# Performance work log

Hardware: AMD Instinct MI355X
Metric: run time of the kernel (lower is better)

The kernel has to match this reference:

```python
import jax, jax.numpy as jnp
import numpy as np

N_NODES = 20000
N_EDGES = 320000
IN_DIM = 256
HIDDEN = 256
OUT_DIM = 128
N_LAYERS = 3
N_GROUPS = 4
EXP_PER_GROUP = 2
N_EXPERTS = N_GROUPS * EXP_PER_GROUP
TOP_K = 2


def setup_inputs() -> dict:
    key = jax.random.key(0)
    ks = jax.random.split(key, 12)
    d = HIDDEN
    r = 2 * d  # router/expert input dim: concat(node, neighbor-mean)
    x = jax.random.normal(ks[0], (N_NODES, IN_DIM), dtype=jnp.float32)
    edge_index = jax.random.randint(ks[1], (2, N_EDGES), 0, N_NODES, dtype=jnp.int32)
    s = 0.05
    Wg = jax.random.normal(ks[2], (N_LAYERS, r, N_GROUPS), dtype=jnp.float32) * s
    We = jax.random.normal(ks[3], (N_LAYERS, r, N_EXPERTS), dtype=jnp.float32) * s
    Ww = jax.random.normal(ks[4], (N_LAYERS, r, d), dtype=jnp.float32) * s
    W1 = jax.random.normal(ks[5], (N_LAYERS, N_EXPERTS, r, d), dtype=jnp.float32) * s
    b1 = jnp.zeros((N_LAYERS, N_EXPERTS, d), dtype=jnp.float32)
    W2 = jax.random.normal(ks[6], (N_LAYERS, N_EXPERTS, d, d), dtype=jnp.float32) * s
    b2 = jnp.zeros((N_LAYERS, N_EXPERTS, d), dtype=jnp.float32)
    wc = jax.random.normal(ks[7], (N_LAYERS, r, 1), dtype=jnp.float32) * s
    Wout = jax.random.normal(ks[8], (d, OUT_DIM), dtype=jnp.float32) * s
    return {"x": x, "edge_index": edge_index, "Wg": Wg, "We": We, "Ww": Ww,
            "W1": W1, "b1": b1, "W2": W2, "b2": b2, "wc": wc, "Wout": Wout}


def _moe_layer(h, src, dst, deg, Wg, We, Ww, W1, b1, W2, b2, wc):
    N = h.shape[0]
    # graph message passing: mean aggregation over incoming edges
    agg = jax.ops.segment_sum(h[src], dst, num_segments=N) / deg  # [N, d]
    r = jnp.concatenate([h, agg], axis=-1)  # [N, 2d] combined router input
    # hierarchical routing: group softmax x within-group expert softmax
    gp = jax.nn.softmax(r @ Wg, axis=-1)                                # [N, G]
    ep = jax.nn.softmax((r @ We).reshape(N, N_GROUPS, EXP_PER_GROUP), axis=-1)
    probs = (gp[..., None] * ep).reshape(N, N_EXPERTS)                  # [N, E]
    # top-k gating, renormalized
    topv, topi = jax.lax.top_k(probs, TOP_K)
    gates = jnp.zeros_like(probs).at[jnp.arange(N)[:, None], topi].set(topv)
    gates = gates / (gates.sum(-1, keepdims=True) + 1e-9)              # [N, E]
    # strong experts: per-expert 2-layer MLP, combined by gates
    hid = jax.nn.relu(jnp.einsum('nf,efd->ned', r, W1) + b1[None])      # [N, E, d]
    exp_out = jnp.einsum('ned,edo->neo', hid, W2) + b2[None]            # [N, E, d]
    strong = jnp.einsum('ne,neo->no', gates, exp_out)                   # [N, d]
    # weak shared expert + confidence gate blend
    weak = r @ Ww                                                       # [N, d]
    conf = jax.nn.sigmoid(r @ wc)                                       # [N, 1]
    return jax.nn.relu(conf * strong + (1.0 - conf) * weak)


def reference(x, edge_index, Wg, We, Ww, W1, b1, W2, b2, wc, Wout):
    src, dst = edge_index[0], edge_index[1]
    N = x.shape[0]
    deg = jax.ops.segment_sum(jnp.ones((edge_index.shape[1],), jnp.float32), dst,
                              num_segments=N)
    deg = jnp.maximum(deg, 1.0)[:, None]
    h = x
    for l in range(Wg.shape[0]):  # small fixed layer loop
        h = _moe_layer(h, src, dst, deg, Wg[l], We[l], Ww[l],
                       W1[l], b1[l], W2[l], b2[l], wc[l])
    return h @ Wout
```

## Files before the change

kernel.cpp:

```cpp
#include <hip/hip_runtime.h>

#define NN 20000
#define NEDGE 320000
#define D 256
#define RD 512
#define OD 128
#define NEXP 8
#define NSLOT (2*NN)
#define NODE_BLOCKS 79
#define ASSIGN_BLOCKS 157
#define EXP_BLOCKS 640

typedef unsigned short u16;
typedef __attribute__((ext_vector_type(4))) short short4v;
typedef __attribute__((ext_vector_type(8))) short short8v;
typedef __attribute__((ext_vector_type(16))) float f32x16;

__device__ __forceinline__ void split1(float v, u16& h, u16& m, u16& l) {
    unsigned b = __float_as_uint(v);
    h = (u16)(b >> 16);
    float fh = __uint_as_float(b & 0xffff0000u);
    float r1 = v - fh;
    unsigned b1 = __float_as_uint(r1);
    m = (u16)(b1 >> 16);
    float fm = __uint_as_float(b1 & 0xffff0000u);
    float r2 = r1 - fm;
    l = (u16)(__float_as_uint(r2) >> 16);
}


__global__ void copy_x_zero_cnt_k(const float* __restrict__ x, float* __restrict__ r,
                                  int* __restrict__ cnt) {
    int gid = blockIdx.x * 256 + threadIdx.x;
    int n = gid >> 6;
    int c4 = gid & 63;
    if (gid < NN * (D / 4)) {
        float4 v = reinterpret_cast<const float4*>(x)[gid];
        reinterpret_cast<float4*>(r + (size_t)n * RD)[c4] = v;
    }
    if (gid < NN) cnt[gid] = 0;
}

__global__ void count_edges_k(const int* __restrict__ dst, int* __restrict__ cnt) {
    int e = blockIdx.x * 256 + threadIdx.x;
    if (e < NEDGE) atomicAdd(&cnt[dst[e]], 1);
}

__global__ void block_sums_k(const int* __restrict__ cnt, int* __restrict__ bsum) {
    __shared__ int s[256];
    int i = blockIdx.x * 256 + threadIdx.x;
    s[threadIdx.x] = (i < NN) ? cnt[i] : 0;
    __syncthreads();
    for (int off = 128; off > 0; off >>= 1) {
        if (threadIdx.x < off) s[threadIdx.x] += s[threadIdx.x + off];
        __syncthreads();
    }
    if (threadIdx.x == 0) bsum[blockIdx.x] = s[0];
}

__global__ void scan_bsums_k(int* __restrict__ bsum, int* __restrict__ row_start) {
    if (blockIdx.x == 0 && threadIdx.x == 0) {
        int acc = 0;
        for (int i = 0; i < NODE_BLOCKS; i++) { int t = bsum[i]; bsum[i] = acc; acc += t; }
        row_start[NN] = acc;
    }
}

__global__ void block_scan_k(const int* __restrict__ cnt, const int* __restrict__ bsum,
                             int* __restrict__ row_start, int* __restrict__ cur) {
    __shared__ int s[256];
    int i = blockIdx.x * 256 + threadIdx.x;
    int v = (i < NN) ? cnt[i] : 0;
    s[threadIdx.x] = v;
    __syncthreads();
    for (int off = 1; off < 256; off <<= 1) {
        int t = (threadIdx.x >= off) ? s[threadIdx.x - off] : 0;
        __syncthreads();
        s[threadIdx.x] += t;
        __syncthreads();
    }
    int excl = s[threadIdx.x] - v + bsum[blockIdx.x];
    if (i < NN) { row_start[i] = excl; cur[i] = excl; }
}

__global__ void fill_csr_k(const int* __restrict__ src, const int* __restrict__ dst,
                           int* __restrict__ cur, int* __restrict__ csr_src) {
    int e = blockIdx.x * 256 + threadIdx.x;
    if (e < NEDGE) {
        int pos = atomicAdd(&cur[dst[e]], 1);
        csr_src[pos] = src[e];
    }
}

__global__ void aggregate_k(float* __restrict__ r, const int* __restrict__ row_start,
                            const int* __restrict__ csr_src) {
    int wid = blockIdx.x * 4 + (threadIdx.x >> 6);
    int lane = threadIdx.x & 63;
    if (wid >= NN) return;
    int beg = row_start[wid], end = row_start[wid + 1];
    float ax = 0.f, ay = 0.f, az = 0.f, aw = 0.f;
    for (int j = beg; j < end; j++) {
        int s = csr_src[j];
        float4 v = reinterpret_cast<const float4*>(r + (size_t)s * RD)[lane];
        ax += v.x; ay += v.y; az += v.z; aw += v.w;
    }
    float deg = (float)((end - beg) > 1 ? (end - beg) : 1);
    float4 o = make_float4(ax / deg, ay / deg, az / deg, aw / deg);
    reinterpret_cast<float4*>(r + (size_t)wid * RD + D)[lane] = o;
}

__global__ void router_k(const float* __restrict__ r, const float* __restrict__ Wg,
                         const float* __restrict__ We, const float* __restrict__ wc,
                         int* __restrict__ node_top, float* __restrict__ node_gate,
                         float* __restrict__ conf) {
    int wid = blockIdx.x * 4 + (threadIdx.x >> 6);
    int lane = threadIdx.x & 63;
    if (wid >= NN) return;

    const float* rrow = r + (size_t)wid * RD;
    float pg[4] = {0, 0, 0, 0};
    float pe[8] = {0, 0, 0, 0, 0, 0, 0, 0};
    float pc = 0.f;
#pragma unroll
    for (int i = 0; i < 8; i++) {
        int k = lane + i * 64;
        float rv = rrow[k];
        float4 wg = *reinterpret_cast<const float4*>(Wg + (size_t)k * 4);
        pg[0] = fmaf(rv, wg.x, pg[0]); pg[1] = fmaf(rv, wg.y, pg[1]);
        pg[2] = fmaf(rv, wg.z, pg[2]); pg[3] = fmaf(rv, wg.w, pg[3]);
        float4 w0 = *reinterpret_cast<const float4*>(We + (size_t)k * 8);
        float4 w1 = *reinterpret_cast<const float4*>(We + (size_t)k * 8 + 4);
        pe[0] = fmaf(rv, w0.x, pe[0]); pe[1] = fmaf(rv, w0.y, pe[1]);
        pe[2] = fmaf(rv, w0.z, pe[2]); pe[3] = fmaf(rv, w0.w, pe[3]);
        pe[4] = fmaf(rv, w1.x, pe[4]); pe[5] = fmaf(rv, w1.y, pe[5]);
        pe[6] = fmaf(rv, w1.z, pe[6]); pe[7] = fmaf(rv, w1.w, pe[7]);
        pc = fmaf(rv, wc[k], pc);
    }
#pragma unroll
    for (int off = 32; off > 0; off >>= 1) {
#pragma unroll
        for (int g = 0; g < 4; g++) pg[g] += __shfl_xor(pg[g], off);
#pragma unroll
        for (int g = 0; g < 8; g++) pe[g] += __shfl_xor(pe[g], off);
        pc += __shfl_xor(pc, off);
    }

    if (lane == 0) {
        float m = fmaxf(fmaxf(pg[0], pg[1]), fmaxf(pg[2], pg[3]));
        float eg[4]; float sg = 0.f;
#pragma unroll
        for (int g = 0; g < 4; g++) { eg[g] = expf(pg[g] - m); sg += eg[g]; }
        float probs[8];
#pragma unroll
        for (int g = 0; g < 4; g++) {
            float a = pe[2 * g], b = pe[2 * g + 1];
            float mm = fmaxf(a, b);
            float ea = expf(a - mm), eb = expf(b - mm);
            float inv = 1.f / (ea + eb);
            float gp = eg[g] / sg;
            probs[2 * g]     = gp * ea * inv;
            probs[2 * g + 1] = gp * eb * inv;
        }
        int i0 = 0; float v0 = probs[0];
#pragma unroll
        for (int j = 1; j < 8; j++) if (probs[j] > v0) { v0 = probs[j]; i0 = j; }
        int i1 = -1; float v1 = -1e30f;
#pragma unroll
        for (int j = 0; j < 8; j++) if (j != i0 && probs[j] > v1) { v1 = probs[j]; i1 = j; }
        float s = v0 + v1 + 1e-9f;
        node_top[2 * wid] = i0;  node_top[2 * wid + 1] = i1;
        node_gate[2 * wid] = v0 / s;  node_gate[2 * wid + 1] = v1 / s;
        conf[wid] = 1.f / (1.f + expf(-pc));
    }
}

__global__ void hist_part_k(const int* __restrict__ node_top, int* __restrict__ part) {
    __shared__ int h[NEXP];
    if (threadIdx.x < NEXP) h[threadIdx.x] = 0;
    __syncthreads();
    int i = blockIdx.x * 256 + threadIdx.x;
    if (i < NSLOT) atomicAdd(&h[node_top[i]], 1);
    __syncthreads();
    if (threadIdx.x < NEXP) part[blockIdx.x * NEXP + threadIdx.x] = h[threadIdx.x];
}

__global__ void scan2_k(const int* __restrict__ part, int* __restrict__ es,
                        int* __restrict__ ecur) {
    __shared__ int tot[NEXP];
    if (threadIdx.x < NEXP) {
        int s = 0;
        for (int b = 0; b < ASSIGN_BLOCKS; b++) s += part[b * NEXP + threadIdx.x];
        tot[threadIdx.x] = s;
        ecur[threadIdx.x] = 0;
    }
    __syncthreads();
    if (threadIdx.x == 0) {
        int acc = 0;
        for (int e = 0; e < NEXP; e++) { es[e] = acc; acc += tot[e]; }
        es[NEXP] = acc;
    }
}

__global__ void fill_experts_k(const int* __restrict__ node_top, const float* __restrict__ node_gate,
                               const int* __restrict__ es, int* __restrict__ ecur,
                               int* __restrict__ slot_node, float* __restrict__ slot_gate,
                               int* __restrict__ node_slot) {
    __shared__ int hcnt[NEXP], hbase[NEXP];
    int tid = threadIdx.x;
    if (tid < NEXP) hcnt[tid] = 0;
    __syncthreads();
    int i = blockIdx.x * 256 + tid;
    int e = 0, local = 0;
    bool act = (i < NSLOT);
    if (act) {
        e = node_top[i];
        local = atomicAdd(&hcnt[e], 1);
    }
    __syncthreads();
    if (tid < NEXP) hbase[tid] = (hcnt[tid] > 0) ? atomicAdd(&ecur[tid], hcnt[tid]) : 0;
    __syncthreads();
    if (act) {
        int slot = es[e] + hbase[e] + local;
        slot_node[slot] = i >> 1;
        slot_gate[slot] = node_gate[i];
        node_slot[i] = slot;
    }
}

__global__ void combine_k(const float* __restrict__ expout, const float* __restrict__ weak,
                          const float* __restrict__ conf, const int* __restrict__ node_slot,
                          float* __restrict__ r) {
    int gid = blockIdx.x * 256 + threadIdx.x;
    if (gid >= NN * (D / 4)) return;
    int n = gid >> 6, c4 = gid & 63;
    int s0 = node_slot[2 * n], s1 = node_slot[2 * n + 1];
    float4 e0 = reinterpret_cast<const float4*>(expout + (size_t)s0 * D)[c4];
    float4 e1 = reinterpret_cast<const float4*>(expout + (size_t)s1 * D)[c4];
    float4 w  = reinterpret_cast<const float4*>(weak + (size_t)n * D)[c4];
    float cf = conf[n], cg = 1.f - cf;
    float4 o;
    o.x = fmaxf(cf * (e0.x + e1.x) + cg * w.x, 0.f);
    o.y = fmaxf(cf * (e0.y + e1.y) + cg * w.y, 0.f);
    o.z = fmaxf(cf * (e0.z + e1.z) + cg * w.z, 0.f);
    o.w = fmaxf(cf * (e0.w + e1.w) + cg * w.w, 0.f);
    reinterpret_cast<float4*>(r + (size_t)n * RD)[c4] = o;
}

__device__ __forceinline__ void btile_one(const float* __restrict__ src,
                                          u16* __restrict__ dH, u16* __restrict__ dM,
                                          u16* __restrict__ dL, int K, int N, int gid) {
    int l = gid & 63;
    int tile = gid >> 6;
    int K16 = K >> 4;
    int kb = tile % K16;
    int t2 = tile / K16;
    int N32 = N >> 5;
    int nb = t2 % N32;
    int mat = t2 / N32;
    int kbase = (kb << 4) + ((l >> 5) << 3);
    int n = (nb << 5) + (l & 31);
    const float* s = src + ((size_t)mat * K + kbase) * N + n;
    short8v vh, vm, vl;
#pragma unroll
    for (int j = 0; j < 8; j++) {
        u16 hh, mm, ll;
        split1(s[(size_t)j * N], hh, mm, ll);
        vh[j] = (short)hh; vm[j] = (short)mm; vl[j] = (short)ll;
    }
    size_t o = (size_t)gid * 8;
    *reinterpret_cast<short8v*>(dH + o) = vh;
    *reinterpret_cast<short8v*>(dM + o) = vm;
    *reinterpret_cast<short8v*>(dL + o) = vl;
}

__global__ void btile_k(const float* __restrict__ src, u16* __restrict__ dH,
                        u16* __restrict__ dM, u16* __restrict__ dL,
                        int K, int N, int total) {
    int gid = blockIdx.x * 256 + threadIdx.x;
    if (gid >= total) return;
    btile_one(src, dH, dM, dL, K, N, gid);
}

__global__ void btile3_k(const float* __restrict__ s1, u16* __restrict__ aH,
                         u16* __restrict__ aM, u16* __restrict__ aL,
                         const float* __restrict__ s2, u16* __restrict__ bH,
                         u16* __restrict__ bM, u16* __restrict__ bL,
                         const float* __restrict__ s3, u16* __restrict__ cH,
                         u16* __restrict__ cM, u16* __restrict__ cL) {
    int gid = blockIdx.x * 256 + threadIdx.x;
    if (gid < 131072) {
        btile_one(s1, aH, aM, aL, RD, D, gid);
    } else if (gid < 131072 + 65536) {
        btile_one(s2, bH, bM, bL, D, D, gid - 131072);
    } else if (gid < 131072 + 65536 + 16384) {
        btile_one(s3, cH, cM, cL, RD, D, gid - 131072 - 65536);
    }
}

template <int MODE>
__global__ __launch_bounds__(256, 5) void gemm_mfma(
    const float* __restrict__ A, int lda,
    const u16* __restrict__ BH, const u16* __restrict__ BM,
    const u16* __restrict__ BL,
    const float* __restrict__ bias,
    float* __restrict__ C, int ldc,
    const int* __restrict__ es,
    const int* __restrict__ slot_node,
    const float* __restrict__ slot_gate,
    int M, int N, int K,
    const u16* __restrict__ VH, const u16* __restrict__ VM,
    const u16* __restrict__ VL, float* __restrict__ Cw,
    int weak_base, int Mw) {
    constexpr int PL2 = 1024;
    __shared__ u16 sA[3 * PL2];

    int tid = threadIdx.x;
    int row0, valid_rows;
    bool isweak = false;
    if (MODE == 0) {
        row0 = blockIdx.x * 64;
        valid_rows = M - row0; if (valid_rows > 64) valid_rows = 64;
    } else if (MODE == 1 && (int)blockIdx.x >= weak_base) {
        isweak = true;
        row0 = ((int)blockIdx.x - weak_base) * 64;
        valid_rows = Mw - row0; if (valid_rows > 64) valid_rows = 64;
        if (valid_rows <= 0) return;
        BH = VH; BM = VM; BL = VL;
        C = Cw;
    } else {
        int bx = blockIdx.x, acc0 = 0, expert = -1, mt = 0;
        row0 = 0; valid_rows = 0;
        for (int e = 0; e < NEXP; e++) {
            int c = es[e + 1] - es[e];
            int t = (c + 63) >> 6;
            if (bx < acc0 + t) {
                expert = e; mt = bx - acc0; row0 = es[e] + (mt << 6);
                valid_rows = c - (mt << 6); if (valid_rows > 64) valid_rows = 64;
                break;
            }
            acc0 += t;
        }
        if (expert < 0) return;
        int bo = expert * N * K;
        BH += bo; BM += bo; BL += bo;
        bias += expert * D;
    }
    int ncol0 = blockIdx.y * 128;

    int srow = tid >> 2;
    int koff = (tid & 3) * 4;
    int grow;
    {
        int i0 = row0 + srow;
        if (MODE == 1 && !isweak) {
            i0 = i0 < NSLOT ? i0 : NSLOT - 1;
            grow = slot_node[i0];
        } else if (MODE == 2) {
            grow = i0 < M ? i0 : M - 1;
        } else if (MODE == 1) {
            grow = i0 < Mw ? i0 : Mw - 1;
        } else {
            grow = i0 < M ? i0 : M - 1;
        }
    }
    const float* pA = A + (size_t)grow * lda + koff;
    int woff = ((srow >> 5) * 2 + (koff >> 3)) * 256 + (srow & 31) * 8 + (koff & 4);

    int lane = tid & 63;
    int wave = tid >> 6;
    int wr = (wave & 1) * 32;
    int wc = (wave >> 1) * 64;
    int fl = lane & 31;
    int K16 = K >> 4;
    int nb0 = (ncol0 + wc) >> 5;
    int tbase0 = nb0 * K16 * 512 + lane * 8;
    int tbase1 = (nb0 + 1) * K16 * 512 + lane * 8;
    int roff = ((wr >> 5) * 2 + (lane >> 5)) * 256 + fl * 8;

    f32x16 acc0 = {};
    f32x16 acc1 = {};

    for (int kt = 0; kt < K; kt += 16) {
        float4 av = *reinterpret_cast<const float4*>(pA + kt);
        int ko = (kt >> 4) * 512;
        short8v bH0 = *reinterpret_cast<const short8v*>(BH + tbase0 + ko);
        short8v bM0 = *reinterpret_cast<const short8v*>(BM + tbase0 + ko);
        short8v bL0 = *reinterpret_cast<const short8v*>(BL + tbase0 + ko);
        short8v bH1 = *reinterpret_cast<const short8v*>(BH + tbase1 + ko);
        short8v bM1 = *reinterpret_cast<const short8v*>(BM + tbase1 + ko);
        short8v bL1 = *reinterpret_cast<const short8v*>(BL + tbase1 + ko);
        __syncthreads();
        {
            u16 h0, m0, l0, h1, m1, l1, h2, m2, l2, h3, m3, l3;
            split1(av.x, h0, m0, l0);
            split1(av.y, h1, m1, l1);
            split1(av.z, h2, m2, l2);
            split1(av.w, h3, m3, l3);
            short4v hv = {(short)h0, (short)h1, (short)h2, (short)h3};
            short4v mv = {(short)m0, (short)m1, (short)m2, (short)m3};
            short4v lv = {(short)l0, (short)l1, (short)l2, (short)l3};
            *reinterpret_cast<short4v*>(&sA[0 * PL2 + woff]) = hv;
            *reinterpret_cast<short4v*>(&sA[1 * PL2 + woff]) = mv;
            *reinterpret_cast<short4v*>(&sA[2 * PL2 + woff]) = lv;
        }
        __syncthreads();
        short8v aH = *reinterpret_cast<const short8v*>(&sA[0 * PL2 + roff]);
        short8v aM = *reinterpret_cast<const short8v*>(&sA[1 * PL2 + roff]);
        short8v aL = *reinterpret_cast<const short8v*>(&sA[2 * PL2 + roff]);
#define MFMA_ACC(d, a, b) d = __builtin_amdgcn_mfma_f32_32x32x16_bf16(a, b, d, 0, 0, 0)
        MFMA_ACC(acc0, aH, bH0); MFMA_ACC(acc0, aH, bM0);
        MFMA_ACC(acc0, aM, bH0); MFMA_ACC(acc0, aH, bL0);
        MFMA_ACC(acc0, aM, bM0); MFMA_ACC(acc0, aL, bH0);
        MFMA_ACC(acc1, aH, bH1); MFMA_ACC(acc1, aH, bM1);
        MFMA_ACC(acc1, aM, bH1); MFMA_ACC(acc1, aH, bL1);
        MFMA_ACC(acc1, aM, bM1); MFMA_ACC(acc1, aL, bH1);
#undef MFMA_ACC
    }

    int fh = lane >> 5;
#pragma unroll
    for (int j = 0; j < 2; j++) {
        const f32x16& a = j ? acc1 : acc0;
        int colg = ncol0 + wc + j * 32 + fl;
        float bv = (MODE != 0 && !isweak) ? bias[colg] : 0.f;
#pragma unroll
        for (int rg = 0; rg < 16; rg++) {
            int lrow = wr + (rg & 3) + 8 * (rg >> 2) + 4 * fh;
            if (lrow >= valid_rows) continue;
            int growo = row0 + lrow;
            float v = a[rg] + bv;
            if (MODE == 1 && !isweak) {
                v = fmaxf(v, 0.f);
            } else if (MODE == 2) {
                v *= slot_gate[growo];
            }
            C[(size_t)growo * ldc + colg] = v;
        }
    }
}

extern "C" void kernel_launch(void* const* d_in, const int* in_sizes, int n_in,
                              void* d_out, int out_size, void* d_ws, size_t ws_size,
                              hipStream_t stream) {
    (void)in_sizes; (void)n_in; (void)out_size; (void)ws_size;
    const float* x    = (const float*)d_in[0];
    const int*   ei   = (const int*)d_in[1];
    const float* Wg   = (const float*)d_in[2];
    const float* We   = (const float*)d_in[3];
    const float* Ww   = (const float*)d_in[4];
    const float* W1   = (const float*)d_in[5];
    const float* b1   = (const float*)d_in[6];
    const float* W2   = (const float*)d_in[7];
    const float* b2   = (const float*)d_in[8];
    const float* wcp  = (const float*)d_in[9];
    const float* Wout = (const float*)d_in[10];
    float* out = (float*)d_out;

    char* p = (char*)d_ws;
    auto alloc = [&](size_t bytes) -> char* {
        char* q = p; p += (bytes + 255) & ~(size_t)255; return q;
    };
    int*   cnt       = (int*)alloc((size_t)NN * 4);
    int*   row_start = (int*)alloc((size_t)(NN + 1) * 4);
    int*   cur       = (int*)alloc((size_t)NN * 4);
    int*   bsum      = (int*)alloc(128 * 4);
    int*   csr_src   = (int*)alloc((size_t)NEDGE * 4);
    float* r         = (float*)alloc((size_t)NN * RD * 4);
    float* hid       = (float*)alloc((size_t)NSLOT * D * 4);
    float* expout    = (float*)alloc((size_t)NSLOT * D * 4);
    float* weak      = (float*)alloc((size_t)NN * D * 4);
    float* conf      = (float*)alloc((size_t)NN * 4);
    int*   node_top  = (int*)alloc((size_t)2 * NN * 4);
    float* node_gate = (float*)alloc((size_t)2 * NN * 4);
    int*   node_slot = (int*)alloc((size_t)2 * NN * 4);
    int*   slot_node = (int*)alloc((size_t)NSLOT * 4);
    float* slot_gate = (float*)alloc((size_t)NSLOT * 4);
    int*   part      = (int*)alloc((size_t)ASSIGN_BLOCKS * NEXP * 4);
    int*   es        = (int*)alloc(64 * 4);
    int*   ecur      = (int*)alloc(64 * 4);
    u16* w1tH = (u16*)alloc((size_t)NEXP * D * RD * 2);
    u16* w1tM = (u16*)alloc((size_t)NEXP * D * RD * 2);
    u16* w1tL = (u16*)alloc((size_t)NEXP * D * RD * 2);
    u16* w2tH = (u16*)alloc((size_t)NEXP * D * D * 2);
    u16* w2tM = (u16*)alloc((size_t)NEXP * D * D * 2);
    u16* w2tL = (u16*)alloc((size_t)NEXP * D * D * 2);
    u16* wwtH = (u16*)alloc((size_t)D * RD * 2);
    u16* wwtM = (u16*)alloc((size_t)D * RD * 2);
    u16* wwtL = (u16*)alloc((size_t)D * RD * 2);
    u16* wotH = (u16*)alloc((size_t)OD * D * 2);
    u16* wotM = (u16*)alloc((size_t)OD * D * 2);
    u16* wotL = (u16*)alloc((size_t)OD * D * 2);

    const int* srcp = ei;
    const int* dstp = ei + NEDGE;
    const int EB = (NEDGE + 255) / 256;

    copy_x_zero_cnt_k<<<5000, 256, 0, stream>>>(x, r, cnt);
    count_edges_k<<<EB, 256, 0, stream>>>(dstp, cnt);
    block_sums_k<<<NODE_BLOCKS, 256, 0, stream>>>(cnt, bsum);
    scan_bsums_k<<<1, 64, 0, stream>>>(bsum, row_start);
    block_scan_k<<<NODE_BLOCKS, 256, 0, stream>>>(cnt, bsum, row_start, cur);
    fill_csr_k<<<EB, 256, 0, stream>>>(srcp, dstp, cur, csr_src);
    btile_k<<<16, 256, 0, stream>>>(Wout, wotH, wotM, wotL, D, OD, 4096);

    for (int l = 0; l < 3; l++) {
        btile3_k<<<832, 256, 0, stream>>>(
            W1 + (size_t)l * NEXP * RD * D, w1tH, w1tM, w1tL,
            W2 + (size_t)l * NEXP * D * D,  w2tH, w2tM, w2tL,
            Ww + (size_t)l * RD * D,        wwtH, wwtM, wwtL);
        aggregate_k<<<5000, 256, 0, stream>>>(r, row_start, csr_src);
        router_k<<<5000, 256, 0, stream>>>(r,
            Wg + (size_t)l * RD * 4, We + (size_t)l * RD * 8, wcp + (size_t)l * RD,
            node_top, node_gate, conf);
        hist_part_k<<<ASSIGN_BLOCKS, 256, 0, stream>>>(node_top, part);
        scan2_k<<<1, 64, 0, stream>>>(part, es, ecur);
        fill_experts_k<<<ASSIGN_BLOCKS, 256, 0, stream>>>(node_top, node_gate, es, ecur,
                                                          slot_node, slot_gate, node_slot);
        gemm_mfma<1><<<dim3(EXP_BLOCKS + 313, 2), 256, 0, stream>>>(
            r, RD, w1tH, w1tM, w1tL, b1 + (size_t)l * NEXP * D, hid, D,
            es, slot_node, slot_gate, NSLOT, D, RD,
            wwtH, wwtM, wwtL, weak, EXP_BLOCKS, NN);
        gemm_mfma<2><<<dim3(EXP_BLOCKS, 2), 256, 0, stream>>>(
            hid, D, w2tH, w2tM, w2tL, b2 + (size_t)l * NEXP * D, expout, D,
            es, slot_node, slot_gate, NSLOT, D, D,
            nullptr, nullptr, nullptr, nullptr, 1 << 30, 0);
        combine_k<<<5000, 256, 0, stream>>>(expout, weak, conf, node_slot, r);
    }
    gemm_mfma<0><<<dim3(313, 1), 256, 0, stream>>>(
        r, RD, wotH, wotM, wotL, nullptr, out, OD,
        nullptr, nullptr, nullptr, NN, OD, D,
        nullptr, nullptr, nullptr, nullptr, 1 << 30, 0);
}
```

Baseline: 813.5 us.

## Fuse aggregation with router and batch all-layer weight splitting up front

Merges the neighbor-mean aggregation and router kernels so the router works from register-resident node and aggregate values instead of re-reading the row from global memory. When the workspace is large enough, it also converts the weights of all three layers into bf16 split tiles with one up-front launch instead of one per layer. The aim is to cut launch count and memory traffic. The cost is a larger workspace, plus a fallback path that keeps the per-layer conversion when space is short.

```diff
diff --git a/kernel.cpp b/kernel.cpp
--- a/kernel.cpp
+++ b/kernel.cpp
@@ -92,11 +92,16 @@
     }
 }
 
-__global__ void aggregate_k(float* __restrict__ r, const int* __restrict__ row_start,
-                            const int* __restrict__ csr_src) {
+__global__ void agg_router_k(float* __restrict__ r, const int* __restrict__ row_start,
+                             const int* __restrict__ csr_src,
+                             const float* __restrict__ Wg, const float* __restrict__ We,
+                             const float* __restrict__ wc,
+                             int* __restrict__ node_top, float* __restrict__ node_gate,
+                             float* __restrict__ conf) {
     int wid = blockIdx.x * 4 + (threadIdx.x >> 6);
     int lane = threadIdx.x & 63;
     if (wid >= NN) return;
+
     int beg = row_start[wid], end = row_start[wid + 1];
     float ax = 0.f, ay = 0.f, az = 0.f, aw = 0.f;
     for (int j = beg; j < end; j++) {
@@ -105,26 +110,14 @@
         ax += v.x; ay += v.y; az += v.z; aw += v.w;
     }
     float deg = (float)((end - beg) > 1 ? (end - beg) : 1);
-    float4 o = make_float4(ax / deg, ay / deg, az / deg, aw / deg);
-    reinterpret_cast<float4*>(r + (size_t)wid * RD + D)[lane] = o;
-}
-
-__global__ void router_k(const float* __restrict__ r, const float* __restrict__ Wg,
-                         const float* __restrict__ We, const float* __restrict__ wc,
-                         int* __restrict__ node_top, float* __restrict__ node_gate,
-                         float* __restrict__ conf) {
-    int wid = blockIdx.x * 4 + (threadIdx.x >> 6);
-    int lane = threadIdx.x & 63;
-    if (wid >= NN) return;
-
-    const float* rrow = r + (size_t)wid * RD;
+    float4 av = make_float4(ax / deg, ay / deg, az / deg, aw / deg);
+    reinterpret_cast<float4*>(r + (size_t)wid * RD + D)[lane] = av;
+
+    float4 hv = reinterpret_cast<const float4*>(r + (size_t)wid * RD)[lane];
     float pg[4] = {0, 0, 0, 0};
     float pe[8] = {0, 0, 0, 0, 0, 0, 0, 0};
     float pc = 0.f;
-#pragma unroll
-    for (int i = 0; i < 8; i++) {
-        int k = lane + i * 64;
-        float rv = rrow[k];
+    auto step = [&](int k, float rv) {
         float4 wg = *reinterpret_cast<const float4*>(Wg + (size_t)k * 4);
         pg[0] = fmaf(rv, wg.x, pg[0]); pg[1] = fmaf(rv, wg.y, pg[1]);
         pg[2] = fmaf(rv, wg.z, pg[2]); pg[3] = fmaf(rv, wg.w, pg[3]);
@@ -135,7 +128,12 @@
         pe[4] = fmaf(rv, w1.x, pe[4]); pe[5] = fmaf(rv, w1.y, pe[5]);
         pe[6] = fmaf(rv, w1.z, pe[6]); pe[7] = fmaf(rv, w1.w, pe[7]);
         pc = fmaf(rv, wc[k], pc);
-    }
+    };
+    int k0 = 4 * lane;
+    step(k0 + 0, hv.x); step(k0 + 1, hv.y); step(k0 + 2, hv.z); step(k0 + 3, hv.w);
+    int k1 = D + 4 * lane;
+    step(k1 + 0, av.x); step(k1 + 1, av.y); step(k1 + 2, av.z); step(k1 + 3, av.w);
+
 #pragma unroll
     for (int off = 32; off > 0; off >>= 1) {
 #pragma unroll
@@ -294,6 +292,34 @@
         btile_one(s2, bH, bM, bL, D, D, gid - 131072);
     } else if (gid < 131072 + 65536 + 16384) {
         btile_one(s3, cH, cM, cL, RD, D, gid - 131072 - 65536);
+    }
+}
+
+__global__ void btile_all_k(const float* __restrict__ W1, u16* __restrict__ aH,
+                            u16* __restrict__ aM, u16* __restrict__ aL,
+                            const float* __restrict__ W2, u16* __restrict__ bH,
+                            u16* __restrict__ bM, u16* __restrict__ bL,
+                            const float* __restrict__ Ww, u16* __restrict__ cH,
+                            u16* __restrict__ cM, u16* __restrict__ cL,
+                            const float* __restrict__ Wout, u16* __restrict__ oH,
+                            u16* __restrict__ oM, u16* __restrict__ oL) {
+    int gid = blockIdx.x * 256 + threadIdx.x;
+    const int L1 = 131072, L2 = 65536, L3 = 16384, PER = L1 + L2 + L3;
+    if (gid < 3 * PER) {
+        int l = gid / PER, g = gid - l * PER;
+        if (g < L1) {
+            btile_one(W1 + (size_t)l * NEXP * RD * D, aH + (size_t)l * L1 * 8,
+                      aM + (size_t)l * L1 * 8, aL + (size_t)l * L1 * 8, RD, D, g);
+        } else if (g < L1 + L2) {
+            btile_one(W2 + (size_t)l * NEXP * D * D, bH + (size_t)l * L2 * 8,
+                      bM + (size_t)l * L2 * 8, bL + (size_t)l * L2 * 8, D, D, g - L1);
+        } else {
+            btile_one(Ww + (size_t)l * RD * D, cH + (size_t)l * L3 * 8,
+                      cM + (size_t)l * L3 * 8, cL + (size_t)l * L3 * 8, RD, D,
+                      g - L1 - L2);
+        }
+    } else if (gid < 3 * PER + 4096) {
+        btile_one(Wout, oH, oM, oL, D, OD, gid - 3 * PER);
     }
 }
 
@@ -442,7 +468,7 @@
 extern "C" void kernel_launch(void* const* d_in, const int* in_sizes, int n_in,
                               void* d_out, int out_size, void* d_ws, size_t ws_size,
                               hipStream_t stream) {
-    (void)in_sizes; (void)n_in; (void)out_size; (void)ws_size;
+    (void)in_sizes; (void)n_in; (void)out_size;
     const float* x    = (const float*)d_in[0];
     const int*   ei   = (const int*)d_in[1];
     const float* Wg   = (const float*)d_in[2];
@@ -478,18 +504,27 @@
     int*   part      = (int*)alloc((size_t)ASSIGN_BLOCKS * NEXP * 4);
     int*   es        = (int*)alloc(64 * 4);
     int*   ecur      = (int*)alloc(64 * 4);
-    u16* w1tH = (u16*)alloc((size_t)NEXP * D * RD * 2);
-    u16* w1tM = (u16*)alloc((size_t)NEXP * D * RD * 2);
-    u16* w1tL = (u16*)alloc((size_t)NEXP * D * RD * 2);
-    u16* w2tH = (u16*)alloc((size_t)NEXP * D * D * 2);
-    u16* w2tM = (u16*)alloc((size_t)NEXP * D * D * 2);
-    u16* w2tL = (u16*)alloc((size_t)NEXP * D * D * 2);
-    u16* wwtH = (u16*)alloc((size_t)D * RD * 2);
-    u16* wwtM = (u16*)alloc((size_t)D * RD * 2);
-    u16* wwtL = (u16*)alloc((size_t)D * RD * 2);
-    u16* wotH = (u16*)alloc((size_t)OD * D * 2);
-    u16* wotM = (u16*)alloc((size_t)OD * D * 2);
-    u16* wotL = (u16*)alloc((size_t)OD * D * 2);
+
+    const size_t SZ1 = (size_t)NEXP * D * RD;
+    const size_t SZ2 = (size_t)NEXP * D * D;
+    const size_t SZW = (size_t)RD * D;
+    const size_t SZO = (size_t)OD * D;
+    size_t used = (size_t)(p - (char*)d_ws);
+    size_t need3 = 3 * 3 * (SZ1 + SZ2 + SZW) * 2 + 3 * SZO * 2 + 16384;
+    bool all3 = used + need3 <= ws_size;
+    int nl = all3 ? 3 : 1;
+    u16* w1tH = (u16*)alloc((size_t)nl * SZ1 * 2);
+    u16* w1tM = (u16*)alloc((size_t)nl * SZ1 * 2);
+    u16* w1tL = (u16*)alloc((size_t)nl * SZ1 * 2);
+    u16* w2tH = (u16*)alloc((size_t)nl * SZ2 * 2);
+    u16* w2tM = (u16*)alloc((size_t)nl * SZ2 * 2);
+    u16* w2tL = (u16*)alloc((size_t)nl * SZ2 * 2);
+    u16* wwtH = (u16*)alloc((size_t)nl * SZW * 2);
+    u16* wwtM = (u16*)alloc((size_t)nl * SZW * 2);
+    u16* wwtL = (u16*)alloc((size_t)nl * SZW * 2);
+    u16* wotH = (u16*)alloc(SZO * 2);
+    u16* wotM = (u16*)alloc(SZO * 2);
+    u16* wotL = (u16*)alloc(SZO * 2);
 
     const int* srcp = ei;
     const int* dstp = ei + NEDGE;
@@ -501,15 +536,27 @@
     scan_bsums_k<<<1, 64, 0, stream>>>(bsum, row_start);
     block_scan_k<<<NODE_BLOCKS, 256, 0, stream>>>(cnt, bsum, row_start, cur);
     fill_csr_k<<<EB, 256, 0, stream>>>(srcp, dstp, cur, csr_src);
-    btile_k<<<16, 256, 0, stream>>>(Wout, wotH, wotM, wotL, D, OD, 4096);
+    if (all3) {
+        btile_all_k<<<2512, 256, 0, stream>>>(W1, w1tH, w1tM, w1tL,
+                                              W2, w2tH, w2tM, w2tL,
+                                              Ww, wwtH, wwtM, wwtL,
+                                              Wout, wotH, wotM, wotL);
+    } else {
+        btile_k<<<16, 256, 0, stream>>>(Wout, wotH, wotM, wotL, D, OD, 4096);
+    }
 
     for (int l = 0; l < 3; l++) {
-        btile3_k<<<832, 256, 0, stream>>>(
-            W1 + (size_t)l * NEXP * RD * D, w1tH, w1tM, w1tL,
-            W2 + (size_t)l * NEXP * D * D,  w2tH, w2tM, w2tL,
-            Ww + (size_t)l * RD * D,        wwtH, wwtM, wwtL);
-        aggregate_k<<<5000, 256, 0, stream>>>(r, row_start, csr_src);
-        router_k<<<5000, 256, 0, stream>>>(r,
+        if (!all3) {
+            btile3_k<<<832, 256, 0, stream>>>(
+                W1 + (size_t)l * NEXP * RD * D, w1tH, w1tM, w1tL,
+                W2 + (size_t)l * NEXP * D * D,  w2tH, w2tM, w2tL,
+                Ww + (size_t)l * RD * D,        wwtH, wwtM, wwtL);
+        }
+        size_t o1 = all3 ? (size_t)l * SZ1 : 0;
+        size_t o2 = all3 ? (size_t)l * SZ2 : 0;
+        size_t ow = all3 ? (size_t)l * SZW : 0;
+
+        agg_router_k<<<5000, 256, 0, stream>>>(r, row_start, csr_src,
             Wg + (size_t)l * RD * 4, We + (size_t)l * RD * 8, wcp + (size_t)l * RD,
             node_top, node_gate, conf);
         hist_part_k<<<ASSIGN_BLOCKS, 256, 0, stream>>>(node_top, part);
@@ -517,11 +564,11 @@
         fill_experts_k<<<ASSIGN_BLOCKS, 256, 0, stream>>>(node_top, node_gate, es, ecur,
                                                           slot_node, slot_gate, node_slot);
         gemm_mfma<1><<<dim3(EXP_BLOCKS + 313, 2), 256, 0, stream>>>(
-            r, RD, w1tH, w1tM, w1tL, b1 + (size_t)l * NEXP * D, hid, D,
+            r, RD, w1tH + o1, w1tM + o1, w1tL + o1, b1 + (size_t)l * NEXP * D, hid, D,
             es, slot_node, slot_gate, NSLOT, D, RD,
-            wwtH, wwtM, wwtL, weak, EXP_BLOCKS, NN);
+            wwtH + ow, wwtM + ow, wwtL + ow, weak, EXP_BLOCKS, NN);
         gemm_mfma<2><<<dim3(EXP_BLOCKS, 2), 256, 0, stream>>>(
-            hid, D, w2tH, w2tM, w2tL, b2 + (size_t)l * NEXP * D, expout, D,
+            hid, D, w2tH + o2, w2tM + o2, w2tL + o2, b2 + (size_t)l * NEXP * D, expout, D,
             es, slot_node, slot_gate, NSLOT, D, D,
             nullptr, nullptr, nullptr, nullptr, 1 << 30, 0);
         combine_k<<<5000, 256, 0, stream>>>(expout, weak, conf, node_slot, r);
```

Result: slower. 839.4 us (median of 3 runs) (+3.2%).
